# Optimization experiments

Measured on AMD Instinct MI355X. Metric: run time of the kernel, lower is better.

The kernel has to match this reference:

```python
import jax, jax.numpy as jnp
import numpy as np

KH = KW = 3  # deformable conv kernel
PAD = 1


def _bilinear_group(img, py, px):
    """img: [Cg,H,W]; py,px: [K,H,W] float sampling coords. Zero padding outside."""
    H, W = img.shape[-2], img.shape[-1]
    y0 = jnp.floor(py).astype(jnp.int32)
    x0 = jnp.floor(px).astype(jnp.int32)
    y1, x1 = y0 + 1, x0 + 1
    wy = py - y0.astype(py.dtype)
    wx = px - x0.astype(px.dtype)

    def g(yi, xi):
        yc = jnp.clip(yi, 0, H - 1)
        xc = jnp.clip(xi, 0, W - 1)
        v = img[:, yc, xc]  # [Cg,K,H,W]
        m = ((yi >= 0) & (yi < H) & (xi >= 0) & (xi < W)).astype(img.dtype)
        return v * m[None]

    return (g(y0, x0) * ((1 - wy) * (1 - wx))[None]
            + g(y0, x1) * ((1 - wy) * wx)[None]
            + g(y1, x0) * (wy * (1 - wx))[None]
            + g(y1, x1) * (wy * wx)[None])  # [Cg,K,H,W]


def reference(x, wh_pred, w_off, b_off, w_d, b_d):
    B, C, H, W = x.shape
    G = w_off.shape[0]          # deformable groups (= n_anchors)
    Cg = C // G
    K = KH * KW
    # grouped 1x1 conv: per anchor group, 2 -> 18 channels
    wh = wh_pred.reshape(B, G, 2, H, W)
    off = jnp.einsum('bgchw,goc->bgohw', wh, w_off) + b_off.reshape(G, 2 * K)[None, :, :, None, None]
    off = off.reshape(B, G, K, 2, H, W)  # channel layout: (dy, dx) per kernel tap
    # base sampling grid: p(h,w,k) = (h - PAD + kh, w - PAD + kw), stride 1
    ky, kx = jnp.meshgrid(jnp.arange(KH), jnp.arange(KW), indexing='ij')
    by = (ky.reshape(K) - PAD).astype(x.dtype)[:, None, None] + jnp.arange(H, dtype=x.dtype)[None, :, None]
    bx = (kx.reshape(K) - PAD).astype(x.dtype)[:, None, None] + jnp.arange(W, dtype=x.dtype)[None, None, :]
    py = off[:, :, :, 0] + by[None, None]  # [B,G,K,H,W]
    px = off[:, :, :, 1] + bx[None, None]
    xg = x.reshape(B, G, Cg, H, W)
    sample = jax.vmap(jax.vmap(_bilinear_group))(xg, py, px)  # [B,G,Cg,K,H,W]
    wd = w_d.reshape(w_d.shape[0], G, Cg, K)
    out = jnp.einsum('bgckhw,ogck->bohw', sample, wd) + b_d[None, :, None, None]
    return out


def setup_inputs() -> dict:
    key = jax.random.key(0)
    k = jax.random.split(key, 5)
    B, C, H, W, G = 8, 256, 64, 64, 4
    Co = 256
    return {
        'x': jax.random.normal(k[0], (B, C, H, W), jnp.float32),
        'wh_pred': jax.random.normal(k[1], (B, 2 * G, H, W), jnp.float32),
        'w_off': jax.random.normal(k[2], (G, 18, 2), jnp.float32) * 0.01,
        'b_off': jnp.zeros((2 * 9 * G,), jnp.float32),
        'w_d': jax.random.normal(k[3], (Co, C, 3, 3), jnp.float32) * (1.0 / np.sqrt(C * 9)),
        'b_d': jnp.zeros((Co,), jnp.float32),
    }
```

## Files before the change

### kernel.cpp

```cpp
#include <hip/hip_runtime.h>

typedef __attribute__((ext_vector_type(8))) short bh8;
typedef __attribute__((ext_vector_type(16))) float f16v;
typedef __attribute__((ext_vector_type(4))) unsigned int u32x4;

#define NTHR 512

__device__ __forceinline__ unsigned int f2bf(float f) {
    unsigned int u = __builtin_bit_cast(unsigned int, f);
    u += 0x7FFFu + ((u >> 16) & 1u);
    return u >> 16;
}
__device__ __forceinline__ float bflo(unsigned int d) {
    return __builtin_bit_cast(float, d << 16);
}
__device__ __forceinline__ float bfhi(unsigned int d) {
    return __builtin_bit_cast(float, d & 0xFFFF0000u);
}

__global__ __launch_bounds__(256) void transpose_x_kernel(
    const float* __restrict__ x, unsigned short* __restrict__ xt) {
    __shared__ float tile[64 * 65];
    const int bid = blockIdx.x;
    const int cq = bid & 3;
    const int h  = (bid >> 2) & 63;
    const int b  = bid >> 8;
    const int tid = threadIdx.x;
    const int w = tid & 63, ci = tid >> 6;
    #pragma unroll
    for (int c0 = 0; c0 < 64; c0 += 4)
        tile[(c0 + ci) * 65 + w] =
            x[(((size_t)b * 256 + cq * 64 + c0 + ci) * 64 + h) * 64 + w];
    __syncthreads();
    const int c2 = tid & 63, w2q = tid >> 6;
    #pragma unroll
    for (int w0 = 0; w0 < 64; w0 += 4) {
        int ww = w0 + w2q;
        xt[(((size_t)b * 64 + h) * 64 + ww) * 256 + cq * 64 + c2] =
            (unsigned short)f2bf(tile[c2 * 65 + ww]);
    }
}

__global__ __launch_bounds__(256) void pack_w16_kernel(const float* __restrict__ w_d,
                                                       bh8* __restrict__ bp) {
    __shared__ float ldw[32 * 145];
    const int cc = blockIdx.x >> 3;
    const int nb = blockIdx.x & 7;
    const int tid = threadIdx.x;
    for (int i = tid; i < 32 * 144; i += 256) {
        int oi = i / 144, j = i - oi * 144;
        ldw[oi * 145 + j] = w_d[(size_t)(nb * 32 + oi) * 2304 + cc * 144 + j];
    }
    __syncthreads();
    for (int u = tid; u < 9 * 64; u += 256) {
        int tt = u >> 6, ll = u & 63;
        int col = ll & 31, hi2 = ll >> 5;
        bh8 v;
        #pragma unroll
        for (int e = 0; e < 8; ++e)
            v[e] = (short)f2bf(ldw[col * 145 + (hi2 * 8 + e) * 9 + tt]);
        bp[((size_t)(cc * 9 + tt) * 8 + nb) * 64 + ll] = v;
    }
}

struct PK { float w00, w01, w10, w11; int A00, A01, sb; };

__global__ __launch_bounds__(NTHR, 4) void featadapt_mfma(
    const unsigned short* __restrict__ xt,
    const float* __restrict__ wh_pred,
    const float* __restrict__ w_off,
    const float* __restrict__ b_off,
    const float* __restrict__ b_d,
    const bh8* __restrict__ bp,
    float* __restrict__ out)
{
    extern __shared__ unsigned char lds[];
    unsigned char* samp = lds;
    unsigned char* tile = lds + 18432;
    float* whs  = (float*)(lds + 29472);
    float* woff = (float*)(lds + 31520);
    float* boff = (float*)(lds + 32096);

    const int tid  = threadIdx.x;
    const int orig = blockIdx.x;
    const int bid  = (orig & 7) * 64 + (orig >> 3);
    const int h = bid & 63;
    const int b = bid >> 6;

    {
        int j = tid >> 6, p = tid & 63;
        whs[p * 8 + j] = wh_pred[(((size_t)b * 8 + j) * 64 + h) * 64 + p];
    }
    if (tid < 144) woff[tid] = w_off[tid];
    else if (tid < 216) boff[tid - 144] = b_off[tid - 144];

    const char* xtb = (const char*)xt + (size_t)b * (64 * 64 * 512);

    auto slotsrc = [&](int s) -> int {
        int cell = s >> 1, j = s & 1;
        int r = cell / 69, c = cell - r * 69;
        int gy = min(max(h - 2 + r, 0), 63);
        int gx = min(max(c - 2, 0), 63);
        int od = j ^ (((c >> 2) + r) & 1);
        return (gy * 64 + gx) * 512 + od * 16;
    };
    const int sg0 = slotsrc(tid);
    const int sg1 = (tid < 178) ? slotsrc(512 + tid) : 0;
    unsigned char* const ld0 = tile + tid * 16;
    unsigned char* const ld1 = tile + 8192 + tid * 16;

    const int l  = tid & 63;
    const int wv = tid >> 6;
    const int arow = l & 31, hi = l >> 5;
    const int ab0 = arow * 288 + hi * 16;
    const int ab1 = ab0 + 32 * 288;
    const int asw = (arow & 7) << 4;

    const int pM = wv * 8 + (l >> 3), tM = l & 7;
    const int pE = wv * 8 + (l >> 1);

    auto calcpk = [&](int p, int tap, int g, PK& S) {
        float wh0 = whs[p * 8 + 2 * g], wh1 = whs[p * 8 + 2 * g + 1];
        int oy = 2 * tap, ox = oy + 1;
        float offy = wh0 * woff[(g * 18 + oy) * 2] + wh1 * woff[(g * 18 + oy) * 2 + 1] + boff[g * 18 + oy];
        float offx = wh0 * woff[(g * 18 + ox) * 2] + wh1 * woff[(g * 18 + ox) * 2 + 1] + boff[g * 18 + ox];
        int ky = tap / 3, kx = tap - ky * 3;
        float py = offy + (float)(ky - 1 + h);
        float px = offx + (float)(kx - 1 + p);
        float fy = floorf(py), fx = floorf(px);
        int y0 = (int)fy, x0 = (int)fx;
        float wy = py - fy, wx = px - fx;
        float my0 = (y0 >= 0 && y0 < 64) ? 1.f : 0.f;
        float my1 = (y0 >= -1 && y0 < 63) ? 1.f : 0.f;
        float mx0 = (x0 >= 0 && x0 < 64) ? 1.f : 0.f;
        float mx1 = (x0 >= -1 && x0 < 63) ? 1.f : 0.f;
        S.w00 = (1.f - wy) * (1.f - wx) * my0 * mx0;
        S.w01 = (1.f - wy) * wx * my0 * mx1;
        S.w10 = wy * (1.f - wx) * my1 * mx0;
        S.w11 = wy * wx * my1 * mx1;
        int r0 = y0 - (h - 2);
        int c0 = x0 + 2, c1 = c0 + 1;
        S.A00 = (r0 * 69 + c0) * 32 + ((((c0 >> 2) + r0) & 1) << 4);
        S.A01 = (r0 * 69 + c1) * 32 + ((((c1 >> 2) + r0) & 1) << 4);
        S.sb  = (p * 288 + tap * 32) ^ ((p & 7) << 4);
    };

    auto sample_oct = [&](const PK& S, int oct) {
        int ox4 = oct << 4;
        u32x4 q00 = *(const u32x4*)(tile + (S.A00 ^ ox4));
        u32x4 q01 = *(const u32x4*)(tile + (S.A01 ^ ox4));
        u32x4 q10 = *(const u32x4*)(tile + (((S.A00 + 2208) ^ 16) ^ ox4));
        u32x4 q11 = *(const u32x4*)(tile + (((S.A01 + 2208) ^ 16) ^ ox4));
        unsigned int ow[4];
        #pragma unroll
        for (int j = 0; j < 4; ++j) {
            float sx = bflo(q00[j]) * S.w00 + bflo(q01[j]) * S.w01
                     + bflo(q10[j]) * S.w10 + bflo(q11[j]) * S.w11;
            float sy = bfhi(q00[j]) * S.w00 + bfhi(q01[j]) * S.w01
                     + bfhi(q10[j]) * S.w10 + bfhi(q11[j]) * S.w11;
            ow[j] = (__builtin_bit_cast(unsigned int, sx) >> 16)
                  | (__builtin_bit_cast(unsigned int, sy) & 0xFFFF0000u);
        }
        u32x4 o4 = {ow[0], ow[1], ow[2], ow[3]};
        *(u32x4*)(samp + (S.sb ^ ox4)) = o4;
    };

    f16v acc0, acc1;
    #pragma unroll
    for (int r = 0; r < 16; ++r) { acc0[r] = 0.f; acc1[r] = 0.f; }

    {
        u32x4 t0 = *(const u32x4*)(xtb + sg0);
        u32x4 t1;
        if (tid < 178) t1 = *(const u32x4*)(xtb + sg1);
        *(u32x4*)ld0 = t0;
        if (tid < 178) *(u32x4*)ld1 = t1;
    }
    __syncthreads();

    PK s0, s1;
    for (int cc = 0; cc < 16; ++cc) {
        if ((cc & 3) == 0) {
            int g = cc >> 2;
            calcpk(pM, tM, g, s0);
            if (l < 16) calcpk(pE, 8, g, s1);
        }
        u32x4 n0, n1;
        if (cc < 15) {
            const int off = (cc + 1) * 32;
            n0 = *(const u32x4*)(xtb + sg0 + off);
            if (tid < 178) n1 = *(const u32x4*)(xtb + sg1 + off);
        }

        sample_oct(s0, 0);
        sample_oct(s0, 1);
        if (l < 16) sample_oct(s1, l & 1);
        __syncthreads();

        const bh8* bpc = bp + ((size_t)cc * 9 * 8 + wv) * 64 + l;
        __builtin_amdgcn_s_setprio(1);
        #pragma unroll
        for (int tt = 0; tt < 9; ++tt) {
            bh8 a0 = *(const bh8*)(samp + ((ab0 + tt * 32) ^ asw));
            bh8 a1 = *(const bh8*)(samp + ((ab1 + tt * 32) ^ asw));
            bh8 bw = bpc[(size_t)tt * 512];
            acc0 = __builtin_amdgcn_mfma_f32_32x32x16_bf16(a0, bw, acc0, 0, 0, 0);
            acc1 = __builtin_amdgcn_mfma_f32_32x32x16_bf16(a1, bw, acc1, 0, 0, 0);
        }
        __builtin_amdgcn_s_setprio(0);

        if (cc < 15) {
            *(u32x4*)ld0 = n0;
            if (tid < 178) *(u32x4*)ld1 = n1;
        }
        __syncthreads();
    }

    const int o = wv * 32 + arow;
    const float bd = b_d[o];
    const size_t ob = (((size_t)b * 256 + o) * 64 + h) * 64;
    #pragma unroll
    for (int q = 0; q < 4; ++q) {
        float4 s4a = make_float4(acc0[4 * q + 0] + bd, acc0[4 * q + 1] + bd,
                                 acc0[4 * q + 2] + bd, acc0[4 * q + 3] + bd);
        *(float4*)&out[ob + hi * 4 + q * 8] = s4a;
        float4 s4b = make_float4(acc1[4 * q + 0] + bd, acc1[4 * q + 1] + bd,
                                 acc1[4 * q + 2] + bd, acc1[4 * q + 3] + bd);
        *(float4*)&out[ob + 32 + hi * 4 + q * 8] = s4b;
    }
}

extern "C" void kernel_launch(void* const* d_in, const int* in_sizes, int n_in,
                              void* d_out, int out_size, void* d_ws, size_t ws_size,
                              hipStream_t stream) {
    const float* x     = (const float*)d_in[0];
    const float* whp   = (const float*)d_in[1];
    const float* w_off = (const float*)d_in[2];
    const float* b_off = (const float*)d_in[3];
    const float* w_d   = (const float*)d_in[4];
    const float* b_d   = (const float*)d_in[5];
    float* out = (float*)d_out;

    unsigned short* xt = (unsigned short*)d_ws;
    bh8* bp = (bh8*)((char*)d_ws + (size_t)8 * 64 * 64 * 256 * 2);

    hipLaunchKernelGGL(transpose_x_kernel, dim3(2048), dim3(256), 0, stream, x, xt);
    hipLaunchKernelGGL(pack_w16_kernel, dim3(128), dim3(256), 0, stream, w_d, bp);
    hipLaunchKernelGGL(featadapt_mfma, dim3(512), dim3(NTHR), 32384, stream,
                       xt, whp, w_off, b_off, b_d, bp, out);
}
```

Before: 86.69 us.

## Switch to fp16 packed bilinear math and double-buffer sample/tile LDS

Replaces bf16 storage and fp32 scalar bilinear blending with fp16 storage and packed half2 FMAs, using the f16 MFMA variant. Double-buffers the input tile and the sampled-patch LDS, so sampling for chunk cc runs in the same barrier interval as the MFMAs for chunk cc-1, removing one barrier per iteration. LDS use roughly doubles to about 62KB per block, which may lower occupancy below the 4 blocks per CU requested in launch bounds. fp16 blending also reduces accumulation precision in the sampling step.

Result: faster. 79.79 us (-8.0%).

```diff
diff --git a/kernel.cpp b/kernel.cpp
--- a/kernel.cpp
+++ b/kernel.cpp
@@ -1,21 +1,21 @@
 #include <hip/hip_runtime.h>
-
-typedef __attribute__((ext_vector_type(8))) short bh8;
+#include <hip/hip_fp16.h>
+
+typedef __attribute__((ext_vector_type(8))) _Float16 h8;
 typedef __attribute__((ext_vector_type(16))) float f16v;
 typedef __attribute__((ext_vector_type(4))) unsigned int u32x4;
 
 #define NTHR 512
 
-__device__ __forceinline__ unsigned int f2bf(float f) {
-    unsigned int u = __builtin_bit_cast(unsigned int, f);
-    u += 0x7FFFu + ((u >> 16) & 1u);
-    return u >> 16;
-}
-__device__ __forceinline__ float bflo(unsigned int d) {
-    return __builtin_bit_cast(float, d << 16);
-}
-__device__ __forceinline__ float bfhi(unsigned int d) {
-    return __builtin_bit_cast(float, d & 0xFFFF0000u);
+__device__ __forceinline__ unsigned short f2h(float f) {
+    _Float16 h = (_Float16)f;
+    return __builtin_bit_cast(unsigned short, h);
+}
+__device__ __forceinline__ __half2 u2h2(unsigned int u) {
+    union { unsigned int u; __half2 h; } cv; cv.u = u; return cv.h;
+}
+__device__ __forceinline__ unsigned int h22u(__half2 h) {
+    union { unsigned int u; __half2 h; } cv; cv.h = h; return cv.u;
 }
 
 __global__ __launch_bounds__(256) void transpose_x_kernel(
@@ -37,12 +37,12 @@
     for (int w0 = 0; w0 < 64; w0 += 4) {
         int ww = w0 + w2q;
         xt[(((size_t)b * 64 + h) * 64 + ww) * 256 + cq * 64 + c2] =
-            (unsigned short)f2bf(tile[c2 * 65 + ww]);
+            f2h(tile[c2 * 65 + ww]);
     }
 }
 
 __global__ __launch_bounds__(256) void pack_w16_kernel(const float* __restrict__ w_d,
-                                                       bh8* __restrict__ bp) {
+                                                       h8* __restrict__ bp) {
     __shared__ float ldw[32 * 145];
     const int cc = blockIdx.x >> 3;
     const int nb = blockIdx.x & 7;
@@ -55,15 +55,15 @@
     for (int u = tid; u < 9 * 64; u += 256) {
         int tt = u >> 6, ll = u & 63;
         int col = ll & 31, hi2 = ll >> 5;
-        bh8 v;
+        h8 v;
         #pragma unroll
         for (int e = 0; e < 8; ++e)
-            v[e] = (short)f2bf(ldw[col * 145 + (hi2 * 8 + e) * 9 + tt]);
+            v[e] = (_Float16)ldw[col * 145 + (hi2 * 8 + e) * 9 + tt];
         bp[((size_t)(cc * 9 + tt) * 8 + nb) * 64 + ll] = v;
     }
 }
 
-struct PK { float w00, w01, w10, w11; int A00, A01, sb; };
+struct PK { __half2 W00, W01, W10, W11; int A00, A01, sb; };
 
 __global__ __launch_bounds__(NTHR, 4) void featadapt_mfma(
     const unsigned short* __restrict__ xt,
@@ -71,15 +71,17 @@
     const float* __restrict__ w_off,
     const float* __restrict__ b_off,
     const float* __restrict__ b_d,
-    const bh8* __restrict__ bp,
+    const h8* __restrict__ bp,
     float* __restrict__ out)
 {
     extern __shared__ unsigned char lds[];
-    unsigned char* samp = lds;
-    unsigned char* tile = lds + 18432;
-    float* whs  = (float*)(lds + 29472);
-    float* woff = (float*)(lds + 31520);
-    float* boff = (float*)(lds + 32096);
+    unsigned char* samp0 = lds;
+    unsigned char* samp1 = lds + 18432;
+    unsigned char* tile0 = lds + 36864;
+    unsigned char* tile1 = lds + 47904;
+    float* whs  = (float*)(lds + 58944);
+    float* woff = (float*)(lds + 60992);
+    float* boff = (float*)(lds + 61568);
 
     const int tid  = threadIdx.x;
     const int orig = blockIdx.x;
@@ -106,8 +108,7 @@
     };
     const int sg0 = slotsrc(tid);
     const int sg1 = (tid < 178) ? slotsrc(512 + tid) : 0;
-    unsigned char* const ld0 = tile + tid * 16;
-    unsigned char* const ld1 = tile + 8192 + tid * 16;
+    const int d0 = tid * 16, d1 = 8192 + tid * 16;
 
     const int l  = tid & 63;
     const int wv = tid >> 6;
@@ -134,10 +135,10 @@
         float my1 = (y0 >= -1 && y0 < 63) ? 1.f : 0.f;
         float mx0 = (x0 >= 0 && x0 < 64) ? 1.f : 0.f;
         float mx1 = (x0 >= -1 && x0 < 63) ? 1.f : 0.f;
-        S.w00 = (1.f - wy) * (1.f - wx) * my0 * mx0;
-        S.w01 = (1.f - wy) * wx * my0 * mx1;
-        S.w10 = wy * (1.f - wx) * my1 * mx0;
-        S.w11 = wy * wx * my1 * mx1;
+        S.W00 = __float2half2_rn((1.f - wy) * (1.f - wx) * my0 * mx0);
+        S.W01 = __float2half2_rn((1.f - wy) * wx * my0 * mx1);
+        S.W10 = __float2half2_rn(wy * (1.f - wx) * my1 * mx0);
+        S.W11 = __float2half2_rn(wy * wx * my1 * mx1);
         int r0 = y0 - (h - 2);
         int c0 = x0 + 2, c1 = c0 + 1;
         S.A00 = (r0 * 69 + c0) * 32 + ((((c0 >> 2) + r0) & 1) << 4);
@@ -145,24 +146,24 @@
         S.sb  = (p * 288 + tap * 32) ^ ((p & 7) << 4);
     };
 
-    auto sample_oct = [&](const PK& S, int oct) {
+    auto sample_oct = [&](const PK& S, int oct,
+                          const unsigned char* tb, unsigned char* sp) {
         int ox4 = oct << 4;
-        u32x4 q00 = *(const u32x4*)(tile + (S.A00 ^ ox4));
-        u32x4 q01 = *(const u32x4*)(tile + (S.A01 ^ ox4));
-        u32x4 q10 = *(const u32x4*)(tile + (((S.A00 + 2208) ^ 16) ^ ox4));
-        u32x4 q11 = *(const u32x4*)(tile + (((S.A01 + 2208) ^ 16) ^ ox4));
+        u32x4 q00 = *(const u32x4*)(tb + (S.A00 ^ ox4));
+        u32x4 q01 = *(const u32x4*)(tb + (S.A01 ^ ox4));
+        u32x4 q10 = *(const u32x4*)(tb + (((S.A00 + 2208) ^ 16) ^ ox4));
+        u32x4 q11 = *(const u32x4*)(tb + (((S.A01 + 2208) ^ 16) ^ ox4));
         unsigned int ow[4];
         #pragma unroll
         for (int j = 0; j < 4; ++j) {
-            float sx = bflo(q00[j]) * S.w00 + bflo(q01[j]) * S.w01
-                     + bflo(q10[j]) * S.w10 + bflo(q11[j]) * S.w11;
-            float sy = bfhi(q00[j]) * S.w00 + bfhi(q01[j]) * S.w01
-                     + bfhi(q10[j]) * S.w10 + bfhi(q11[j]) * S.w11;
-            ow[j] = (__builtin_bit_cast(unsigned int, sx) >> 16)
-                  | (__builtin_bit_cast(unsigned int, sy) & 0xFFFF0000u);
+            __half2 s = __hfma2(u2h2(q00[j]), S.W00,
+                        __hfma2(u2h2(q01[j]), S.W01,
+                        __hfma2(u2h2(q10[j]), S.W10,
+                        __hmul2(u2h2(q11[j]), S.W11))));
+            ow[j] = h22u(s);
         }
         u32x4 o4 = {ow[0], ow[1], ow[2], ow[3]};
-        *(u32x4*)(samp + (S.sb ^ ox4)) = o4;
+        *(u32x4*)(sp + (S.sb ^ ox4)) = o4;
     };
 
     f16v acc0, acc1;
@@ -173,8 +174,8 @@
         u32x4 t0 = *(const u32x4*)(xtb + sg0);
         u32x4 t1;
         if (tid < 178) t1 = *(const u32x4*)(xtb + sg1);
-        *(u32x4*)ld0 = t0;
-        if (tid < 178) *(u32x4*)ld1 = t1;
+        *(u32x4*)(tile0 + d0) = t0;
+        if (tid < 178) *(u32x4*)(tile0 + d1) = t1;
     }
     __syncthreads();
 
@@ -192,28 +193,47 @@
             if (tid < 178) n1 = *(const u32x4*)(xtb + sg1 + off);
         }
 
-        sample_oct(s0, 0);
-        sample_oct(s0, 1);
-        if (l < 16) sample_oct(s1, l & 1);
+        const unsigned char* tb = (cc & 1) ? tile1 : tile0;
+        unsigned char* sp = (cc & 1) ? samp1 : samp0;
+        sample_oct(s0, 0, tb, sp);
+        sample_oct(s0, 1, tb, sp);
+        if (l < 16) sample_oct(s1, l & 1, tb, sp);
+
+        if (cc > 0) {
+            const unsigned char* spp = (cc & 1) ? samp0 : samp1;
+            const h8* bpc = bp + ((size_t)(cc - 1) * 9 * 8 + wv) * 64 + l;
+            __builtin_amdgcn_s_setprio(1);
+            #pragma unroll
+            for (int tt = 0; tt < 9; ++tt) {
+                h8 a0 = *(const h8*)(spp + ((ab0 + tt * 32) ^ asw));
+                h8 a1 = *(const h8*)(spp + ((ab1 + tt * 32) ^ asw));
+                h8 bw = bpc[(size_t)tt * 512];
+                acc0 = __builtin_amdgcn_mfma_f32_32x32x16_f16(a0, bw, acc0, 0, 0, 0);
+                acc1 = __builtin_amdgcn_mfma_f32_32x32x16_f16(a1, bw, acc1, 0, 0, 0);
+            }
+            __builtin_amdgcn_s_setprio(0);
+        }
+
+        if (cc < 15) {
+            unsigned char* tn = (cc & 1) ? tile0 : tile1;
+            *(u32x4*)(tn + d0) = n0;
+            if (tid < 178) *(u32x4*)(tn + d1) = n1;
+        }
         __syncthreads();
-
-        const bh8* bpc = bp + ((size_t)cc * 9 * 8 + wv) * 64 + l;
+    }
+
+    {
+        const h8* bpc = bp + ((size_t)15 * 9 * 8 + wv) * 64 + l;
         __builtin_amdgcn_s_setprio(1);
         #pragma unroll
         for (int tt = 0; tt < 9; ++tt) {
-            bh8 a0 = *(const bh8*)(samp + ((ab0 + tt * 32) ^ asw));
-            bh8 a1 = *(const bh8*)(samp + ((ab1 + tt * 32) ^ asw));
-            bh8 bw = bpc[(size_t)tt * 512];
-            acc0 = __builtin_amdgcn_mfma_f32_32x32x16_bf16(a0, bw, acc0, 0, 0, 0);
-            acc1 = __builtin_amdgcn_mfma_f32_32x32x16_bf16(a1, bw, acc1, 0, 0, 0);
+            h8 a0 = *(const h8*)(samp1 + ((ab0 + tt * 32) ^ asw));
+            h8 a1 = *(const h8*)(samp1 + ((ab1 + tt * 32) ^ asw));
+            h8 bw = bpc[(size_t)tt * 512];
+            acc0 = __builtin_amdgcn_mfma_f32_32x32x16_f16(a0, bw, acc0, 0, 0, 0);
+            acc1 = __builtin_amdgcn_mfma_f32_32x32x16_f16(a1, bw, acc1, 0, 0, 0);
         }
         __builtin_amdgcn_s_setprio(0);
-
-        if (cc < 15) {
-            *(u32x4*)ld0 = n0;
-            if (tid < 178) *(u32x4*)ld1 = n1;
-        }
-        __syncthreads();
     }
 
     const int o = wv * 32 + arow;
@@ -242,10 +262,10 @@
     float* out = (float*)d_out;
 
     unsigned short* xt = (unsigned short*)d_ws;
-    bh8* bp = (bh8*)((char*)d_ws + (size_t)8 * 64 * 64 * 256 * 2);
+    h8* bp = (h8*)((char*)d_ws + (size_t)8 * 64 * 64 * 256 * 2);
 
     hipLaunchKernelGGL(transpose_x_kernel, dim3(2048), dim3(256), 0, stream, x, xt);
     hipLaunchKernelGGL(pack_w16_kernel, dim3(128), dim3(256), 0, stream, w_d, bp);
-    hipLaunchKernelGGL(featadapt_mfma, dim3(512), dim3(NTHR), 32384, stream,
+    hipLaunchKernelGGL(featadapt_mfma, dim3(512), dim3(NTHR), 61856, stream,
                        xt, whp, w_off, b_off, b_d, bp, out);
 }
```
